# Optimization experiments

Measured on AMD Instinct MI355X. Metric: run time of the kernel, lower is better.

## Reference

```python
import jax, jax.numpy as jnp
import numpy as np

N_NODES = 500_000
FEAT_DIM = 256
NUM_CLASSES = 128
NUM_SEGMENTS = 2048


def setup_inputs() -> dict:
    key = jax.random.key(0)
    k_h, k_b, k_w1, k_b1, k_w2, k_b2 = jax.random.split(key, 6)
    H = jax.random.normal(k_h, (N_NODES, FEAT_DIM), dtype=jnp.float32)
    batch = jnp.sort(jax.random.randint(k_b, (N_NODES,), 0, NUM_SEGMENTS, dtype=jnp.int64))
    # MLP(feat_dim, feat_dim, num_classes): Linear -> ReLU -> Linear
    s1 = 1.0 / np.sqrt(FEAT_DIM)
    W1 = jax.random.uniform(k_w1, (FEAT_DIM, FEAT_DIM), jnp.float32, -s1, s1)
    b1 = jax.random.uniform(k_b1, (FEAT_DIM,), jnp.float32, -s1, s1)
    W2 = jax.random.uniform(k_w2, (FEAT_DIM, NUM_CLASSES), jnp.float32, -s1, s1)
    b2 = jax.random.uniform(k_b2, (NUM_CLASSES,), jnp.float32, -s1, s1)
    return {"H": H, "batch": batch, "num_segments": NUM_SEGMENTS,
            "W1": W1, "b1": b1, "W2": W2, "b2": b2}


def segment_softmax(x, seg_ids, num_segments):
    # numerically stable softmax over rows sharing the same segment id (dim 0)
    seg_max = jax.ops.segment_max(x, seg_ids, num_segments=num_segments)  # [S, C]
    shifted = x - seg_max[seg_ids]
    ex = jnp.exp(shifted)
    seg_sum = jax.ops.segment_sum(ex, seg_ids, num_segments=num_segments)  # [S, C]
    return ex / seg_sum[seg_ids]


def reference(H, batch, num_segments, W1, b1, W2, b2):
    # MLP projection: feat_dim -> feat_dim -> num_classes
    h = jax.nn.relu(jnp.einsum('nd,df->nf', H, W1) + b1)
    logits = jnp.einsum('nf,fc->nc', h, W2) + b2  # [N, num_classes]
    # discrete=True path: segment-wise softmax keyed by `batch`
    probs = segment_softmax(logits, batch, num_segments)
    return (logits, probs)
```

## Files before the change

kernel.cpp:

```cpp
#include <hip/hip_runtime.h>
#include <hip/hip_bf16.h>

#define N_NODES 500000
#define FEAT 256
#define NCLS 128
#define NSEG 2048

typedef __attribute__((ext_vector_type(8))) short bfrag8;
typedef __attribute__((ext_vector_type(4))) float facc4;

__device__ __forceinline__ unsigned short f2bf(float f) {
    unsigned int u = __float_as_uint(f);
    u += 0x7FFFu + ((u >> 16) & 1u);
    return (unsigned short)(u >> 16);
}

__global__ void prep_kernel(const float* __restrict__ W1, const float* __restrict__ W2,
                            short* __restrict__ W1t, short* __restrict__ W2t) {
    int idx = blockIdx.x * 256 + threadIdx.x;
    if (idx < FEAT * FEAT) {
        int d = idx >> 8, f = idx & 255;
        W1t[f * FEAT + d] = (short)f2bf(W1[idx]);
    }
    if (idx < FEAT * NCLS) {
        int d = idx >> 7, c = idx & 127;
        W2t[c * FEAT + d] = (short)f2bf(W2[idx]);
    }
}

__global__ __launch_bounds__(256, 2)
void mlp_kernel(const float* __restrict__ H, const short* __restrict__ W1t,
                const float* __restrict__ b1, const short* __restrict__ W2t,
                const float* __restrict__ b2, float* __restrict__ logits) {
    __shared__ short hb[4][32 * 256];

    const int tid  = threadIdx.x;
    const int lane = tid & 63;
    const int l15  = lane & 15;
    const int quad = lane >> 4;
    const int wave = tid >> 6;
    const int row0 = blockIdx.x * 128 + wave * 32;
    short* hw = hb[wave];

    const int rg0 = min(row0 + l15,      N_NODES - 1);
    const int rg1 = min(row0 + 16 + l15, N_NODES - 1);
    const float* rA0 = H + (size_t)rg0 * FEAT;
    const float* rA1 = H + (size_t)rg1 * FEAT;

    facc4 acc[2][16];
    #pragma unroll
    for (int rt = 0; rt < 2; ++rt)
        #pragma unroll
        for (int ct = 0; ct < 16; ++ct)
            acc[rt][ct] = (facc4){0.f, 0.f, 0.f, 0.f};

    #pragma unroll
    for (int kk = 0; kk < 8; ++kk) {
        const int kb = kk * 32 + quad * 8;
        float4 lo0 = *reinterpret_cast<const float4*>(rA0 + kb);
        float4 hi0 = *reinterpret_cast<const float4*>(rA0 + kb + 4);
        float4 lo1 = *reinterpret_cast<const float4*>(rA1 + kb);
        float4 hi1 = *reinterpret_cast<const float4*>(rA1 + kb + 4);
        bfrag8 a0, a1;
        a0[0]=(short)f2bf(lo0.x); a0[1]=(short)f2bf(lo0.y); a0[2]=(short)f2bf(lo0.z); a0[3]=(short)f2bf(lo0.w);
        a0[4]=(short)f2bf(hi0.x); a0[5]=(short)f2bf(hi0.y); a0[6]=(short)f2bf(hi0.z); a0[7]=(short)f2bf(hi0.w);
        a1[0]=(short)f2bf(lo1.x); a1[1]=(short)f2bf(lo1.y); a1[2]=(short)f2bf(lo1.z); a1[3]=(short)f2bf(lo1.w);
        a1[4]=(short)f2bf(hi1.x); a1[5]=(short)f2bf(hi1.y); a1[6]=(short)f2bf(hi1.z); a1[7]=(short)f2bf(hi1.w);
        #pragma unroll
        for (int ct = 0; ct < 16; ++ct) {
            bfrag8 b = *reinterpret_cast<const bfrag8*>(&W1t[(ct * 16 + l15) * FEAT + kb]);
            acc[0][ct] = __builtin_amdgcn_mfma_f32_16x16x32_bf16(a0, b, acc[0][ct], 0, 0, 0);
            acc[1][ct] = __builtin_amdgcn_mfma_f32_16x16x32_bf16(a1, b, acc[1][ct], 0, 0, 0);
        }
    }

    #pragma unroll
    for (int ct = 0; ct < 16; ++ct) {
        float bias = b1[ct * 16 + l15];
        int c = ct * 16 + l15;
        #pragma unroll
        for (int rt = 0; rt < 2; ++rt) {
            int rbase = rt * 16 + quad * 4;
            #pragma unroll
            for (int i = 0; i < 4; ++i) {
                float v = fmaxf(acc[rt][ct][i] + bias, 0.f);
                int r = rbase + i;
                int g = (c >> 3) ^ (r & 7);
                hw[r * 256 + g * 8 + (c & 7)] = (short)f2bf(v);
            }
        }
    }

    const int rx = l15 & 7;
    facc4 acc2[2][8];
    #pragma unroll
    for (int rt = 0; rt < 2; ++rt)
        #pragma unroll
        for (int ct = 0; ct < 8; ++ct)
            acc2[rt][ct] = (facc4){0.f, 0.f, 0.f, 0.f};

    #pragma unroll
    for (int kk = 0; kk < 8; ++kk) {
        const int kb = kk * 32 + quad * 8;
        const int gs = ((kb >> 3) ^ rx) << 3;
        bfrag8 a0 = *reinterpret_cast<const bfrag8*>(&hw[l15 * 256 + gs]);
        bfrag8 a1 = *reinterpret_cast<const bfrag8*>(&hw[(16 + l15) * 256 + gs]);
        #pragma unroll
        for (int ct = 0; ct < 8; ++ct) {
            bfrag8 b = *reinterpret_cast<const bfrag8*>(&W2t[(ct * 16 + l15) * FEAT + kb]);
            acc2[0][ct] = __builtin_amdgcn_mfma_f32_16x16x32_bf16(a0, b, acc2[0][ct], 0, 0, 0);
            acc2[1][ct] = __builtin_amdgcn_mfma_f32_16x16x32_bf16(a1, b, acc2[1][ct], 0, 0, 0);
        }
    }

    #pragma unroll
    for (int ct = 0; ct < 8; ++ct) {
        float bias = b2[ct * 16 + l15];
        int c = ct * 16 + l15;
        #pragma unroll
        for (int rt = 0; rt < 2; ++rt) {
            int rbase = row0 + rt * 16 + quad * 4;
            #pragma unroll
            for (int i = 0; i < 4; ++i) {
                int r = rbase + i;
                if (r < N_NODES)
                    logits[(size_t)r * NCLS + c] = acc2[rt][ct][i] + bias;
            }
        }
    }
}

__global__ void seg_sum_kernel(const float* __restrict__ logits,
                               const int* __restrict__ batch,
                               float* __restrict__ Lsum) {
    int seg = blockIdx.x;
    int lo = 0, hi = N_NODES;
    while (lo < hi) { int m = (lo + hi) >> 1; if (batch[m] < seg) lo = m + 1; else hi = m; }
    int start = lo;
    hi = N_NODES;
    while (lo < hi) { int m = (lo + hi) >> 1; if (batch[m] < seg + 1) lo = m + 1; else hi = m; }
    int end = lo;

    int t = threadIdx.x;
    int cg = t & 31;
    int rs = t >> 5;
    float4 s = {0.f, 0.f, 0.f, 0.f};
    for (int r = start + rs; r < end; r += 8) {
        float4 v = *reinterpret_cast<const float4*>(&logits[(size_t)r * NCLS + cg * 4]);
        s.x += __expf(v.x); s.y += __expf(v.y);
        s.z += __expf(v.z); s.w += __expf(v.w);
    }

    __shared__ float4 red[8][32];
    red[rs][cg] = s;
    __syncthreads();
    if (t < 32) {
        float4 a = red[0][t];
        #pragma unroll
        for (int k = 1; k < 8; ++k) {
            float4 b = red[k][t];
            a.x += b.x; a.y += b.y; a.z += b.z; a.w += b.w;
        }
        *reinterpret_cast<float4*>(&Lsum[(size_t)seg * NCLS + t * 4]) = a;
    }
}

__global__ void probs_kernel(const float* __restrict__ logits,
                             const int* __restrict__ batch,
                             const float* __restrict__ Lsum,
                             float* __restrict__ probs) {
    int idx = blockIdx.x * 256 + threadIdx.x;
    int n = idx >> 5;
    if (n >= N_NODES) return;
    int c4 = (idx & 31) << 2;
    int seg = batch[n];
    float4 lg = *reinterpret_cast<const float4*>(&logits[(size_t)n * NCLS + c4]);
    float4 L  = *reinterpret_cast<const float4*>(&Lsum[(size_t)seg * NCLS + c4]);
    float4 p;
    p.x = __expf(lg.x) / L.x; p.y = __expf(lg.y) / L.y;
    p.z = __expf(lg.z) / L.z; p.w = __expf(lg.w) / L.w;
    *reinterpret_cast<float4*>(&probs[(size_t)n * NCLS + c4]) = p;
}

extern "C" void kernel_launch(void* const* d_in, const int* in_sizes, int n_in,
                              void* d_out, int out_size, void* d_ws, size_t ws_size,
                              hipStream_t stream) {
    const float* H     = (const float*)d_in[0];
    const int*   batch = (const int*)d_in[1];
    const float* W1    = (const float*)d_in[3];
    const float* b1    = (const float*)d_in[4];
    const float* W2    = (const float*)d_in[5];
    const float* b2    = (const float*)d_in[6];

    float* out    = (float*)d_out;
    float* logits = out;
    float* probs  = out + (size_t)N_NODES * NCLS;

    char* ws = (char*)d_ws;
    short* W1t  = (short*)ws;
    short* W2t  = (short*)(ws + 131072);
    float* Lsum = (float*)(ws + 131072 + 65536);

    prep_kernel<<<256, 256, 0, stream>>>(W1, W2, W1t, W2t);
    mlp_kernel<<<(N_NODES + 127) / 128, 256, 0, stream>>>(H, W1t, b1, W2t, b2, logits);
    seg_sum_kernel<<<NSEG, 256, 0, stream>>>(logits, batch, Lsum);
    probs_kernel<<<(N_NODES * 32 + 255) / 256, 256, 0, stream>>>(logits, batch, Lsum, probs);
}
```

Baseline: 1.309 ms.

## Shrink MLP tile to 16 rows per wave and use atomic segment sums

The MLP kernel now handles 16 rows per wave instead of 32. This cuts the accumulator registers and LDS per block so that four blocks can be resident per CU, at the cost of reading the weights twice as often per row. The segment-sum kernel no longer runs a per-segment binary search over 2048 blocks. It streams fixed chunks of 256 rows, accumulates runs of equal segment id, and flushes each run with float atomics into a buffer that a new kernel zeroes first. The atomics add contention and make the summation order nondeterministic.

```diff
diff --git a/kernel.cpp b/kernel.cpp
--- a/kernel.cpp
+++ b/kernel.cpp
@@ -28,49 +28,51 @@
     }
 }
 
-__global__ __launch_bounds__(256, 2)
+__global__ void zero_kernel(float4* __restrict__ p) {
+    p[blockIdx.x * 256 + threadIdx.x] = (float4){0.f, 0.f, 0.f, 0.f};
+}
+
+__global__ __launch_bounds__(256, 4)
 void mlp_kernel(const float* __restrict__ H, const short* __restrict__ W1t,
                 const float* __restrict__ b1, const short* __restrict__ W2t,
                 const float* __restrict__ b2, float* __restrict__ logits) {
-    __shared__ short hb[4][32 * 256];
+    __shared__ short hb[4][16 * 256];
 
     const int tid  = threadIdx.x;
     const int lane = tid & 63;
     const int l15  = lane & 15;
     const int quad = lane >> 4;
     const int wave = tid >> 6;
-    const int row0 = blockIdx.x * 128 + wave * 32;
+    const int row0 = blockIdx.x * 64 + wave * 16;
     short* hw = hb[wave];
 
-    const int rg0 = min(row0 + l15,      N_NODES - 1);
-    const int rg1 = min(row0 + 16 + l15, N_NODES - 1);
-    const float* rA0 = H + (size_t)rg0 * FEAT;
-    const float* rA1 = H + (size_t)rg1 * FEAT;
+    const int rg = min(row0 + l15, N_NODES - 1);
+    const float* rA = H + (size_t)rg * FEAT;
 
-    facc4 acc[2][16];
+    bfrag8 af[8];
     #pragma unroll
-    for (int rt = 0; rt < 2; ++rt)
-        #pragma unroll
-        for (int ct = 0; ct < 16; ++ct)
-            acc[rt][ct] = (facc4){0.f, 0.f, 0.f, 0.f};
+    for (int kk = 0; kk < 8; ++kk) {
+        const int kb = kk * 32 + quad * 8;
+        float4 lo = *reinterpret_cast<const float4*>(rA + kb);
+        float4 hi = *reinterpret_cast<const float4*>(rA + kb + 4);
+        bfrag8 a;
+        a[0]=(short)f2bf(lo.x); a[1]=(short)f2bf(lo.y); a[2]=(short)f2bf(lo.z); a[3]=(short)f2bf(lo.w);
+        a[4]=(short)f2bf(hi.x); a[5]=(short)f2bf(hi.y); a[6]=(short)f2bf(hi.z); a[7]=(short)f2bf(hi.w);
+        af[kk] = a;
+    }
+
+    facc4 acc[16];
+    #pragma unroll
+    for (int ct = 0; ct < 16; ++ct)
+        acc[ct] = (facc4){0.f, 0.f, 0.f, 0.f};
 
     #pragma unroll
     for (int kk = 0; kk < 8; ++kk) {
         const int kb = kk * 32 + quad * 8;
-        float4 lo0 = *reinterpret_cast<const float4*>(rA0 + kb);
-        float4 hi0 = *reinterpret_cast<const float4*>(rA0 + kb + 4);
-        float4 lo1 = *reinterpret_cast<const float4*>(rA1 + kb);
-        float4 hi1 = *reinterpret_cast<const float4*>(rA1 + kb + 4);
-        bfrag8 a0, a1;
-        a0[0]=(short)f2bf(lo0.x); a0[1]=(short)f2bf(lo0.y); a0[2]=(short)f2bf(lo0.z); a0[3]=(short)f2bf(lo0.w);
-        a0[4]=(short)f2bf(hi0.x); a0[5]=(short)f2bf(hi0.y); a0[6]=(short)f2bf(hi0.z); a0[7]=(short)f2bf(hi0.w);
-        a1[0]=(short)f2bf(lo1.x); a1[1]=(short)f2bf(lo1.y); a1[2]=(short)f2bf(lo1.z); a1[3]=(short)f2bf(lo1.w);
-        a1[4]=(short)f2bf(hi1.x); a1[5]=(short)f2bf(hi1.y); a1[6]=(short)f2bf(hi1.z); a1[7]=(short)f2bf(hi1.w);
         #pragma unroll
         for (int ct = 0; ct < 16; ++ct) {
             bfrag8 b = *reinterpret_cast<const bfrag8*>(&W1t[(ct * 16 + l15) * FEAT + kb]);
-            acc[0][ct] = __builtin_amdgcn_mfma_f32_16x16x32_bf16(a0, b, acc[0][ct], 0, 0, 0);
-            acc[1][ct] = __builtin_amdgcn_mfma_f32_16x16x32_bf16(a1, b, acc[1][ct], 0, 0, 0);
+            acc[ct] = __builtin_amdgcn_mfma_f32_16x16x32_bf16(af[kk], b, acc[ct], 0, 0, 0);
         }
     }
 
@@ -78,38 +80,31 @@
     for (int ct = 0; ct < 16; ++ct) {
         float bias = b1[ct * 16 + l15];
         int c = ct * 16 + l15;
+        int rbase = quad * 4;
         #pragma unroll
-        for (int rt = 0; rt < 2; ++rt) {
-            int rbase = rt * 16 + quad * 4;
-            #pragma unroll
-            for (int i = 0; i < 4; ++i) {
-                float v = fmaxf(acc[rt][ct][i] + bias, 0.f);
-                int r = rbase + i;
-                int g = (c >> 3) ^ (r & 7);
-                hw[r * 256 + g * 8 + (c & 7)] = (short)f2bf(v);
-            }
+        for (int i = 0; i < 4; ++i) {
+            float v = fmaxf(acc[ct][i] + bias, 0.f);
+            int r = rbase + i;
+            int g = (c >> 3) ^ (r & 7);
+            hw[r * 256 + g * 8 + (c & 7)] = (short)f2bf(v);
         }
     }
 
     const int rx = l15 & 7;
-    facc4 acc2[2][8];
+    facc4 acc2[8];
     #pragma unroll
-    for (int rt = 0; rt < 2; ++rt)
-        #pragma unroll
-        for (int ct = 0; ct < 8; ++ct)
-            acc2[rt][ct] = (facc4){0.f, 0.f, 0.f, 0.f};
+    for (int ct = 0; ct < 8; ++ct)
+        acc2[ct] = (facc4){0.f, 0.f, 0.f, 0.f};
 
     #pragma unroll
     for (int kk = 0; kk < 8; ++kk) {
         const int kb = kk * 32 + quad * 8;
         const int gs = ((kb >> 3) ^ rx) << 3;
-        bfrag8 a0 = *reinterpret_cast<const bfrag8*>(&hw[l15 * 256 + gs]);
-        bfrag8 a1 = *reinterpret_cast<const bfrag8*>(&hw[(16 + l15) * 256 + gs]);
+        bfrag8 a = *reinterpret_cast<const bfrag8*>(&hw[l15 * 256 + gs]);
         #pragma unroll
         for (int ct = 0; ct < 8; ++ct) {
             bfrag8 b = *reinterpret_cast<const bfrag8*>(&W2t[(ct * 16 + l15) * FEAT + kb]);
-            acc2[0][ct] = __builtin_amdgcn_mfma_f32_16x16x32_bf16(a0, b, acc2[0][ct], 0, 0, 0);
-            acc2[1][ct] = __builtin_amdgcn_mfma_f32_16x16x32_bf16(a1, b, acc2[1][ct], 0, 0, 0);
+            acc2[ct] = __builtin_amdgcn_mfma_f32_16x16x32_bf16(a, b, acc2[ct], 0, 0, 0);
         }
     }
 
@@ -117,15 +112,12 @@
     for (int ct = 0; ct < 8; ++ct) {
         float bias = b2[ct * 16 + l15];
         int c = ct * 16 + l15;
+        int rbase = row0 + quad * 4;
         #pragma unroll
-        for (int rt = 0; rt < 2; ++rt) {
-            int rbase = row0 + rt * 16 + quad * 4;
-            #pragma unroll
-            for (int i = 0; i < 4; ++i) {
-                int r = rbase + i;
-                if (r < N_NODES)
-                    logits[(size_t)r * NCLS + c] = acc2[rt][ct][i] + bias;
-            }
+        for (int i = 0; i < 4; ++i) {
+            int r = rbase + i;
+            if (r < N_NODES)
+                logits[(size_t)r * NCLS + c] = acc2[ct][i] + bias;
         }
     }
 }
@@ -133,35 +125,33 @@
 __global__ void seg_sum_kernel(const float* __restrict__ logits,
                                const int* __restrict__ batch,
                                float* __restrict__ Lsum) {
-    int seg = blockIdx.x;
-    int lo = 0, hi = N_NODES;
-    while (lo < hi) { int m = (lo + hi) >> 1; if (batch[m] < seg) lo = m + 1; else hi = m; }
-    int start = lo;
-    hi = N_NODES;
-    while (lo < hi) { int m = (lo + hi) >> 1; if (batch[m] < seg + 1) lo = m + 1; else hi = m; }
-    int end = lo;
-
     int t = threadIdx.x;
     int cg = t & 31;
     int rs = t >> 5;
+    int r0 = blockIdx.x * 256;
+    int rend = min(r0 + 256, N_NODES);
+
     float4 s = {0.f, 0.f, 0.f, 0.f};
-    for (int r = start + rs; r < end; r += 8) {
+    int cur = -1;
+    for (int r = r0 + rs; r < rend; r += 8) {
+        int seg = batch[r];
         float4 v = *reinterpret_cast<const float4*>(&logits[(size_t)r * NCLS + cg * 4]);
+        if (seg != cur) {
+            if (cur >= 0) {
+                float* dst = &Lsum[(size_t)cur * NCLS + cg * 4];
+                atomicAdd(dst + 0, s.x); atomicAdd(dst + 1, s.y);
+                atomicAdd(dst + 2, s.z); atomicAdd(dst + 3, s.w);
+            }
+            cur = seg;
+            s = (float4){0.f, 0.f, 0.f, 0.f};
+        }
         s.x += __expf(v.x); s.y += __expf(v.y);
         s.z += __expf(v.z); s.w += __expf(v.w);
     }
-
-    __shared__ float4 red[8][32];
-    red[rs][cg] = s;
-    __syncthreads();
-    if (t < 32) {
-        float4 a = red[0][t];
-        #pragma unroll
-        for (int k = 1; k < 8; ++k) {
-            float4 b = red[k][t];
-            a.x += b.x; a.y += b.y; a.z += b.z; a.w += b.w;
-        }
-        *reinterpret_cast<float4*>(&Lsum[(size_t)seg * NCLS + t * 4]) = a;
+    if (cur >= 0) {
+        float* dst = &Lsum[(size_t)cur * NCLS + cg * 4];
+        atomicAdd(dst + 0, s.x); atomicAdd(dst + 1, s.y);
+        atomicAdd(dst + 2, s.z); atomicAdd(dst + 3, s.w);
     }
 }
 
@@ -202,7 +192,8 @@
     float* Lsum = (float*)(ws + 131072 + 65536);
 
     prep_kernel<<<256, 256, 0, stream>>>(W1, W2, W1t, W2t);
-    mlp_kernel<<<(N_NODES + 127) / 128, 256, 0, stream>>>(H, W1t, b1, W2t, b2, logits);
-    seg_sum_kernel<<<NSEG, 256, 0, stream>>>(logits, batch, Lsum);
+    zero_kernel<<<(NSEG * NCLS) / (4 * 256), 256, 0, stream>>>((float4*)Lsum);
+    mlp_kernel<<<(N_NODES + 63) / 64, 256, 0, stream>>>(H, W1t, b1, W2t, b2, logits);
+    seg_sum_kernel<<<(N_NODES + 255) / 256, 256, 0, stream>>>(logits, batch, Lsum);
     probs_kernel<<<(N_NODES * 32 + 255) / 256, 256, 0, stream>>>(logits, batch, Lsum, probs);
 }
```

Result: slower. 1.560 ms (+19.1%).
